# Performance work log

Hardware: AMD Instinct MI355X
Metric: run time of the kernel (lower is better)

Reference implementation:

```python
import jax, jax.numpy as jnp
import numpy as np

SEQ_LEN = 16
N_NODES = 64000
N_EDGES = 1024000
FEAT = 16
H1 = 64
H2 = 64
LSTM_DIM = 128
FC1 = 64
FC2 = 3


def setup_inputs() -> dict:
    key = jax.random.key(0)
    ks = jax.random.split(key, 16)
    def w(k, shape, fan_in):
        return (jax.random.normal(k, shape, jnp.float32) / np.float32(np.sqrt(fan_in)))
    return {
        "x": jax.random.normal(ks[0], (N_NODES, FEAT), jnp.float32),
        "edge_attr": jax.random.uniform(ks[1], (N_EDGES, 1), jnp.float32),
        "W1": w(ks[2], (FEAT, H1), FEAT),
        "b1": jnp.zeros((H1,), jnp.float32),
        "W2": w(ks[3], (H1, H2), H1),
        "b2": jnp.zeros((H2,), jnp.float32),
        "W_ih": w(ks[4], (4 * LSTM_DIM, H2), H2),
        "W_hh": w(ks[5], (4 * LSTM_DIM, LSTM_DIM), LSTM_DIM),
        "b_ih": jnp.zeros((4 * LSTM_DIM,), jnp.float32),
        "b_hh": jnp.zeros((4 * LSTM_DIM,), jnp.float32),
        "fw1": w(ks[6], (LSTM_DIM, FC1), LSTM_DIM),
        "fb1": jnp.zeros((FC1,), jnp.float32),
        "fw2": w(ks[7], (FC1, FC2), FC1),
        "fb2": jnp.zeros((FC2,), jnp.float32),
        "edge_index": jax.random.randint(ks[8], (2, N_EDGES), 0, N_NODES, dtype=jnp.int64),
        "batch_size": 8,
    }


def gcn_conv(x, edge_index, ew, W, b):
    # PyG GCNConv with edge_weight: add self-loops (weight 1), symmetric norm.
    n = x.shape[0]
    row, col = edge_index[0], edge_index[1]
    lin = x @ W                                        # [N, H]
    deg = jax.ops.segment_sum(ew, col, num_segments=n) + 1.0  # self-loop weight 1
    dinv = jax.lax.rsqrt(deg)
    norm = dinv[row] * ew * dinv[col]                  # [E]
    agg = jax.ops.segment_sum(norm[:, None] * lin[row], col, num_segments=n)
    agg = agg + lin * (dinv * dinv)[:, None]           # self-loop term: 1/deg
    return agg + b


def lstm_last(x, W_ih, W_hh, b_ih, b_hh):
    # x: [B, T, D]; torch LSTM gate order i, f, g, o. Returns last hidden [B, H].
    B = x.shape[0]
    H = W_hh.shape[1]
    xg = jnp.einsum('btd,gd->btg', x, W_ih) + (b_ih + b_hh)  # [B, T, 4H]
    def step(carry, g_t):
        h, c = carry
        g = g_t + h @ W_hh.T
        i, f, gg, o = jnp.split(g, 4, axis=-1)
        c = jax.nn.sigmoid(f) * c + jax.nn.sigmoid(i) * jnp.tanh(gg)
        h = jax.nn.sigmoid(o) * jnp.tanh(c)
        return (h, c), None
    h0 = jnp.zeros((B, H), x.dtype)
    (h, _), _ = jax.lax.scan(step, (h0, h0), xg.transpose(1, 0, 2))
    return h


def reference(x, edge_attr, W1, b1, W2, b2, W_ih, W_hh, b_ih, b_hh,
              fw1, fb1, fw2, fb2, edge_index, batch_size):
    ew = edge_attr[:, 0]
    out = gcn_conv(x, edge_index, ew, W1, b1)
    out = jax.nn.relu(out)                 # dropout: identity in eval
    out = gcn_conv(out, edge_index, ew, W2, b2)
    out = jax.nn.relu(out)
    out = out.reshape(-1, SEQ_LEN, out.shape[-1])      # [B*S, T, H2]
    h = lstm_last(out, W_ih, W_hh, b_ih, b_hh)          # [B*S, LSTM]
    h = h.reshape(batch_size, -1, LSTM_DIM)             # [B, S, LSTM]
    h = jax.nn.relu(h @ fw1 + fb1)
    logits = h @ fw2 + fb2
    return jax.nn.softmax(logits, axis=2)
```

## Files before the change

kernel.cpp:

```cpp
#include <hip/hip_runtime.h>
#include <hip/hip_bf16.h>
#include <hip/hip_fp16.h>
#include <math.h>

#define NN 64000
#define NE 1024000
#define NB 4000
#define NT 16
#define LROWS 16
#define NBKT 250

typedef __attribute__((ext_vector_type(8))) short short8;
typedef __attribute__((ext_vector_type(4))) float f32x4;

__device__ __forceinline__ float fsigm(float x) {
    return __builtin_amdgcn_rcpf(1.0f + __expf(-x));
}
__device__ __forceinline__ float ftanh(float x) {
    return 1.0f - 2.0f * __builtin_amdgcn_rcpf(1.0f + __expf(2.0f * x));
}
__device__ __forceinline__ unsigned short hbits(float v) {
    __half h = __float2half(v);
    return reinterpret_cast<unsigned short&>(h);
}
__device__ __forceinline__ float hval(unsigned short b) {
    __half h;
    reinterpret_cast<unsigned short&>(h) = b;
    return __half2float(h);
}

__global__ __launch_bounds__(256) void k_zero256(int* __restrict__ p) {
    p[threadIdx.x] = 0;
}

__global__ __launch_bounds__(256) void k_bhist(const int* __restrict__ ei,
                                               int* __restrict__ bcnt) {
    __shared__ int h[256];
    int tid = threadIdx.x;
    h[tid] = 0;
    __syncthreads();
    int base = blockIdx.x * 4096;
    #pragma unroll
    for (int j = 0; j < 16; ++j) {
        int c = ei[NE + base + j * 256 + tid];
        atomicAdd(&h[c >> 8], 1);
    }
    __syncthreads();
    if (tid < NBKT && h[tid]) atomicAdd(&bcnt[tid], h[tid]);
}

__global__ __launch_bounds__(256) void k_bscan(const int* __restrict__ bcnt,
                                               int* __restrict__ bbase,
                                               int* __restrict__ bcur) {
    __shared__ int sm[256];
    int tid = threadIdx.x;
    int v = (tid < NBKT) ? bcnt[tid] : 0;
    sm[tid] = v;
    __syncthreads();
    #pragma unroll
    for (int d = 1; d < 256; d <<= 1) {
        int t = (tid >= d) ? sm[tid - d] : 0;
        __syncthreads();
        sm[tid] += t;
        __syncthreads();
    }
    if (tid < NBKT) { int ex = sm[tid] - v; bbase[tid] = ex; bcur[tid] = ex; }
    if (tid == 255) bbase[NBKT] = sm[255];
}

__global__ __launch_bounds__(256) void k_bin(const int* __restrict__ ei,
                                             const float* __restrict__ ew,
                                             int* __restrict__ bcur,
                                             uint2* __restrict__ binned) {
    __shared__ uint2 stage[4096];
    __shared__ int sm[256];
    __shared__ int lofs[256], lcur[256], ladj[256];
    int tid = threadIdx.x;
    sm[tid] = 0;
    __syncthreads();
    int base = blockIdx.x * 4096;
    int cs[16];
    #pragma unroll
    for (int j = 0; j < 16; ++j) {
        cs[j] = ei[NE + base + j * 256 + tid];
        atomicAdd(&sm[cs[j] >> 8], 1);
    }
    __syncthreads();
    int v = sm[tid];
    #pragma unroll
    for (int d = 1; d < 256; d <<= 1) {
        int t = (tid >= d) ? sm[tid - d] : 0;
        __syncthreads();
        sm[tid] += t;
        __syncthreads();
    }
    int ex = sm[tid] - v;
    lofs[tid] = ex;
    lcur[tid] = ex;
    if (tid < NBKT) ladj[tid] = atomicAdd(&bcur[tid], v) - ex;
    __syncthreads();
    #pragma unroll
    for (int j = 0; j < 16; ++j) {
        int e = base + j * 256 + tid;
        int c = cs[j];
        int b = c >> 8;
        unsigned r = (unsigned)ei[e];
        float wv = ew[e];
        int slot = atomicAdd(&lcur[b], 1);
        stage[slot] = make_uint2(r | ((unsigned)(c & 255) << 16) | ((unsigned)b << 24),
                                 __float_as_uint(wv));
    }
    __syncthreads();
    #pragma unroll
    for (int j = 0; j < 16; ++j) {
        int i = j * 256 + tid;
        uint2 rec = stage[i];
        int b = rec.x >> 24;
        binned[ladj[b] + i] = rec;
    }
}

__global__ __launch_bounds__(256) void k_csr(const uint2* __restrict__ binned,
                                             const int* __restrict__ bbase,
                                             const float* __restrict__ x,
                                             unsigned* __restrict__ edata,
                                             int* __restrict__ off,
                                             float* __restrict__ dinv,
                                             __half* __restrict__ xh) {
    __shared__ int cnt[256];
    __shared__ float sumw[256];
    __shared__ int lcur[256];
    __shared__ int sm[256];
    int tid = threadIdx.x;
    int b = blockIdx.x;
    int s = bbase[b], e1 = bbase[b + 1];
    cnt[tid] = 0;
    sumw[tid] = 0.0f;
    __syncthreads();
    for (int i = s + tid; i < e1; i += 256) {
        uint2 rec = binned[i];
        int nl = (rec.x >> 16) & 255;
        atomicAdd(&cnt[nl], 1);
        atomicAdd(&sumw[nl], __uint_as_float(rec.y));
    }
    __syncthreads();
    int v = cnt[tid];
    sm[tid] = v;
    __syncthreads();
    #pragma unroll
    for (int d = 1; d < 256; d <<= 1) {
        int t = (tid >= d) ? sm[tid - d] : 0;
        __syncthreads();
        sm[tid] += t;
        __syncthreads();
    }
    int ex = sm[tid] - v;
    off[b * 256 + tid] = s + ex;
    float dv = rsqrtf(1.0f + sumw[tid]);
    dinv[b * 256 + tid] = dv;
    sumw[tid] = dv;
    lcur[tid] = ex;
    if (b == 0 && tid == 0) off[NN] = NE;
    __syncthreads();
    for (int i = s + tid; i < e1; i += 256) {
        uint2 rec = binned[i];
        int nl = (rec.x >> 16) & 255;
        int p = atomicAdd(&lcur[nl], 1);
        edata[s + p] = (rec.x & 0xFFFFu) |
                       ((unsigned)hbits(__uint_as_float(rec.y)) << 16);
    }
    size_t nb = (size_t)b * 4096;
    for (int i = tid; i < 4096; i += 256) {
        xh[nb + i] = __float2half(x[nb + i] * sumw[i >> 4]);
    }
}

__global__ __launch_bounds__(256) void k_gather16(const __half* __restrict__ xh,
                                                  const unsigned* __restrict__ edata,
                                                  const int* __restrict__ off,
                                                  const float* __restrict__ dinv,
                                                  __half* __restrict__ aggx) {
    int tid = threadIdx.x;
    int lane = tid & 63;
    int wv = tid >> 6;
    int n = blockIdx.x * 4 + wv;
    int g = lane >> 3;
    int fl = lane & 7;
    const __half2* xh2 = (const __half2*)xh;
    float2 acc = make_float2(0.0f, 0.0f);
    if (g == 0) acc = __half22float2(xh2[((size_t)n << 3) + fl]);
    int s = off[n], e1 = off[n + 1];
    int e = s + g;
    for (; e + 8 < e1; e += 16) {
        unsigned d0 = edata[e];
        unsigned d1 = edata[e + 8];
        float2 l0 = __half22float2(xh2[((size_t)(d0 & 0xFFFFu) << 3) + fl]);
        float2 l1 = __half22float2(xh2[((size_t)(d1 & 0xFFFFu) << 3) + fl]);
        float w0 = hval((unsigned short)(d0 >> 16));
        float w1 = hval((unsigned short)(d1 >> 16));
        acc.x = fmaf(w0, l0.x, acc.x); acc.y = fmaf(w0, l0.y, acc.y);
        acc.x = fmaf(w1, l1.x, acc.x); acc.y = fmaf(w1, l1.y, acc.y);
    }
    if (e < e1) {
        unsigned d0 = edata[e];
        float2 l0 = __half22float2(xh2[((size_t)(d0 & 0xFFFFu) << 3) + fl]);
        float w0 = hval((unsigned short)(d0 >> 16));
        acc.x = fmaf(w0, l0.x, acc.x);
        acc.y = fmaf(w0, l0.y, acc.y);
    }
    acc.x += __shfl_xor(acc.x, 8, 64);
    acc.y += __shfl_xor(acc.y, 8, 64);
    acc.x += __shfl_xor(acc.x, 16, 64);
    acc.y += __shfl_xor(acc.y, 16, 64);
    acc.x += __shfl_xor(acc.x, 32, 64);
    acc.y += __shfl_xor(acc.y, 32, 64);
    if (g == 0) {
        float dn = dinv[n];
        ((__half2*)aggx)[((size_t)n << 3) + fl] = __floats2half2_rn(dn * acc.x, dn * acc.y);
    }
}

__global__ __launch_bounds__(256) void k_wfrag(const float* __restrict__ W_ih,
                                               const float* __restrict__ W_hh,
                                               const float* __restrict__ b_ih,
                                               const float* __restrict__ b_hh,
                                               const float* __restrict__ W1,
                                               const float* __restrict__ W2,
                                               unsigned short* __restrict__ Bus,
                                               float* __restrict__ biasb,
                                               unsigned short* __restrict__ W1f,
                                               unsigned short* __restrict__ W2f) {
    int tid = threadIdx.x;
    int blk = blockIdx.x;
    if (blk < 384) {
        int i = blk * 256 + tid;
        if (i < 192 * 512) {
            int j = i & 7;
            int l = (i >> 3) & 63;
            int ci = i >> 9;
            int ntg = ci & 31;
            int ks = ci >> 5;
            int col = ntg * 16 + (l & 15);
            int k = ks * 32 + ((l >> 4) << 3) + j;
            float w = (k < 64) ? W_ih[col * 64 + k] : W_hh[col * 128 + (k - 64)];
            Bus[i] = hbits(w);
        }
        if (i < 512) biasb[i] = b_ih[i] + b_hh[i];
    } else {
        for (int i = tid; i < 6144; i += 256) {
            if (i < 2048) {
                int j = i & 7, l = (i >> 3) & 63, nt = i >> 9;
                int n = nt * 16 + (l & 15);
                int k = ((l >> 4) << 3) + j;
                W1f[i] = (k < 16) ? hbits(W1[k * 64 + n]) : (unsigned short)0;
            } else {
                int i2 = i - 2048;
                int j = i2 & 7, l = (i2 >> 3) & 63, ci = i2 >> 9;
                int nt = ci & 3, ks = ci >> 2;
                int n = nt * 16 + (l & 15);
                int k = ks * 32 + ((l >> 4) << 3) + j;
                W2f[i2] = hbits(W2[k * 64 + n]);
            }
        }
    }
}

__global__ __launch_bounds__(256) void k_lin2f(const __half* __restrict__ aggx,
                                               const unsigned short* __restrict__ W1f,
                                               const float* __restrict__ b1,
                                               const unsigned short* __restrict__ W2f,
                                               const float* __restrict__ dinv,
                                               __half* __restrict__ linp2) {
    __shared__ unsigned short Ax[4][512];
    __shared__ unsigned short Hd[4][2][512];
    __shared__ unsigned short Ot[64 * 64];
    int tid = threadIdx.x;
    int lane = tid & 63;
    int w = tid >> 6;
    int n0 = blockIdx.x * 64;

    short8 B1[4], B2[8];
    #pragma unroll
    for (int nt = 0; nt < 4; ++nt) B1[nt] = *(const short8*)&W1f[nt * 512 + lane * 8];
    #pragma unroll
    for (int ci = 0; ci < 8; ++ci) B2[ci] = *(const short8*)&W2f[ci * 512 + lane * 8];

    {
        int idx = tid;
        ((unsigned int*)Ax)[(idx >> 7) * 256 + 128 + (idx & 127)] = 0;
        idx += 256;
        ((unsigned int*)Ax)[(idx >> 7) * 256 + 128 + (idx & 127)] = 0;
    }
    {
        int row = tid >> 2, k0 = (tid & 3) * 4;
        uint2 bits = *(const uint2*)(aggx + (size_t)(n0 + row) * 16 + k0);
        unsigned short hv[4] = {(unsigned short)(bits.x & 0xFFFF), (unsigned short)(bits.x >> 16),
                                (unsigned short)(bits.y & 0xFFFF), (unsigned short)(bits.y >> 16)};
        int wq = row >> 4, m = row & 15;
        #pragma unroll
        for (int d = 0; d < 4; ++d) {
            int k = k0 + d;
            Ax[wq][(((k >> 3) << 4) + m) * 8 + (k & 7)] = hv[d];
        }
    }
    __syncthreads();

    short8 a = *(const short8*)&Ax[w][lane * 8];
    f32x4 acc[4];
    #pragma unroll
    for (int nt = 0; nt < 4; ++nt) acc[nt] = (f32x4){0.f, 0.f, 0.f, 0.f};
    #pragma unroll
    for (int nt = 0; nt < 4; ++nt)
        acc[nt] = __builtin_amdgcn_mfma_f32_16x16x32_f16(a, B1[nt], acc[nt], 0, 0, 0);

    int rb = (lane >> 4) * 4;
    #pragma unroll
    for (int nt = 0; nt < 4; ++nt) {
        int col = nt * 16 + (lane & 15);
        float bc = b1[col];
        #pragma unroll
        for (int q = 0; q < 4; ++q) {
            float hv = fmaxf(acc[nt][q] + bc, 0.0f);
            int row = rb + q;
            Hd[w][col >> 5][((((col & 31) >> 3) << 4) + row) * 8 + (col & 7)] = hbits(hv);
        }
    }
    short8 a0 = *(const short8*)&Hd[w][0][lane * 8];
    short8 a1 = *(const short8*)&Hd[w][1][lane * 8];
    f32x4 c2[4];
    #pragma unroll
    for (int nt = 0; nt < 4; ++nt) c2[nt] = (f32x4){0.f, 0.f, 0.f, 0.f};
    #pragma unroll
    for (int nt = 0; nt < 4; ++nt)
        c2[nt] = __builtin_amdgcn_mfma_f32_16x16x32_f16(a0, B2[nt], c2[nt], 0, 0, 0);
    #pragma unroll
    for (int nt = 0; nt < 4; ++nt)
        c2[nt] = __builtin_amdgcn_mfma_f32_16x16x32_f16(a1, B2[4 + nt], c2[nt], 0, 0, 0);

    float dv[4];
    #pragma unroll
    for (int q = 0; q < 4; ++q) dv[q] = dinv[n0 + w * 16 + rb + q];
    #pragma unroll
    for (int nt = 0; nt < 4; ++nt) {
        int col = nt * 16 + (lane & 15);
        #pragma unroll
        for (int q = 0; q < 4; ++q) {
            Ot[(w * 16 + rb + q) * 64 + col] = hbits(c2[nt][q] * dv[q]);
        }
    }
    __syncthreads();
    {
        int row = tid >> 2, c0 = (tid & 3) * 16;
        short8 v0 = *(const short8*)&Ot[row * 64 + c0];
        short8 v1 = *(const short8*)&Ot[row * 64 + c0 + 8];
        *(short8*)&linp2[(size_t)(n0 + row) * 64 + c0] = v0;
        *(short8*)&linp2[(size_t)(n0 + row) * 64 + c0 + 8] = v1;
    }
}

__global__ __launch_bounds__(256) void k_gather(const __half* __restrict__ linp,
                                                const unsigned* __restrict__ edata,
                                                const int* __restrict__ off,
                                                const float* __restrict__ dinv,
                                                const float* __restrict__ bvec,
                                                __half* __restrict__ agg) {
    int tid = threadIdx.x;
    int lane = tid & 63;
    int wv = tid >> 6;
    int n = blockIdx.x * 4 + wv;
    int hf = lane >> 5;
    int fl = lane & 31;
    const __half2* lp2 = (const __half2*)linp;
    float2 acc = make_float2(0.0f, 0.0f);
    if (hf == 0) {
        acc = __half22float2(lp2[((size_t)n << 5) + fl]);
    }
    int s = off[n], e1 = off[n + 1];
    int e = s + hf;
    for (; e + 6 < e1; e += 8) {
        unsigned d0 = edata[e];
        unsigned d1 = edata[e + 2];
        unsigned d2 = edata[e + 4];
        unsigned d3 = edata[e + 6];
        float2 l0 = __half22float2(lp2[((size_t)(d0 & 0xFFFFu) << 5) + fl]);
        float2 l1 = __half22float2(lp2[((size_t)(d1 & 0xFFFFu) << 5) + fl]);
        float2 l2 = __half22float2(lp2[((size_t)(d2 & 0xFFFFu) << 5) + fl]);
        float2 l3 = __half22float2(lp2[((size_t)(d3 & 0xFFFFu) << 5) + fl]);
        float w0 = hval((unsigned short)(d0 >> 16));
        float w1 = hval((unsigned short)(d1 >> 16));
        float w2 = hval((unsigned short)(d2 >> 16));
        float w3 = hval((unsigned short)(d3 >> 16));
        acc.x = fmaf(w0, l0.x, acc.x); acc.y = fmaf(w0, l0.y, acc.y);
        acc.x = fmaf(w1, l1.x, acc.x); acc.y = fmaf(w1, l1.y, acc.y);
        acc.x = fmaf(w2, l2.x, acc.x); acc.y = fmaf(w2, l2.y, acc.y);
        acc.x = fmaf(w3, l3.x, acc.x); acc.y = fmaf(w3, l3.y, acc.y);
    }
    for (; e < e1; e += 2) {
        unsigned d0 = edata[e];
        float2 l0 = __half22float2(lp2[((size_t)(d0 & 0xFFFFu) << 5) + fl]);
        float w0 = hval((unsigned short)(d0 >> 16));
        acc.x = fmaf(w0, l0.x, acc.x);
        acc.y = fmaf(w0, l0.y, acc.y);
    }
    acc.x += __shfl_xor(acc.x, 32, 64);
    acc.y += __shfl_xor(acc.y, 32, 64);
    if (hf == 0) {
        float dn = dinv[n];
        float ox = fmaxf(fmaf(dn, acc.x, bvec[fl * 2]), 0.0f);
        float oy = fmaxf(fmaf(dn, acc.y, bvec[fl * 2 + 1]), 0.0f);
        ((__half2*)agg)[((size_t)n << 5) + fl] = __floats2half2_rn(ox, oy);
    }
}

__global__ __launch_bounds__(512, 2) void k_lstm(const unsigned short* __restrict__ seq,
                                                 const unsigned short* __restrict__ Bus,
                                                 const float* __restrict__ biasb,
                                                 float* __restrict__ hout) {
    __shared__ unsigned short Aus[6 * 512];
    int tid = threadIdx.x;
    int lane = tid & 63;
    int w = tid >> 6;
    int b0 = blockIdx.x * LROWS;

    int u = w * 16 + (lane & 15);
    int rbase = (lane >> 4) * 4;
    float bI = biasb[u], bF = biasb[128 + u], bG = biasb[256 + u], bO = biasb[384 + u];
    float cst[4] = {0.0f, 0.0f, 0.0f, 0.0f};

    short8 Bf[24];
    #pragma unroll
    for (int ks = 0; ks < 6; ++ks) {
        #pragma unroll
        for (int g = 0; g < 4; ++g) {
            int ci = ks * 32 + 8 * g + w;
            Bf[ks * 4 + g] = *(const short8*)&Bus[(size_t)ci * 512 + lane * 8];
        }
    }

    for (int i = tid; i < 1024; i += 512) ((unsigned int*)Aus)[512 + i] = 0;
    {
        int i0 = tid * 2;
        int row = i0 >> 6, k0 = i0 & 63;
        unsigned v = *(const unsigned*)&seq[((size_t)(b0 + row) * NT + 0) * 64 + k0];
        int ks = k0 >> 5, kr = k0 & 31;
        Aus[ks * 512 + (((kr >> 3) << 4) + row) * 8 + (kr & 7)] = (unsigned short)v;
        kr = (k0 + 1) & 31; ks = (k0 + 1) >> 5;
        Aus[ks * 512 + (((kr >> 3) << 4) + row) * 8 + (kr & 7)] = (unsigned short)(v >> 16);
    }
    __syncthreads();

    for (int t = 0; t < NT; ++t) {
        f32x4 acc[4];
        #pragma unroll
        for (int g = 0; g < 4; ++g) acc[g] = (f32x4){0.f, 0.f, 0.f, 0.f};
        #pragma unroll
        for (int ks = 0; ks < 6; ++ks) {
            short8 ah = *(const short8*)&Aus[ks * 512 + lane * 8];
            #pragma unroll
            for (int g = 0; g < 4; ++g)
                acc[g] = __builtin_amdgcn_mfma_f32_16x16x32_f16(ah, Bf[ks * 4 + g], acc[g], 0, 0, 0);
        }
        __syncthreads();

        if (t == NT - 1) {
            #pragma unroll
            for (int q = 0; q < 4; ++q) {
                float nc = fsigm(acc[1][q] + bF) * cst[q]
                         + fsigm(acc[0][q] + bI) * ftanh(acc[2][q] + bG);
                cst[q] = nc;
                float hv = fsigm(acc[3][q] + bO) * ftanh(nc);
                hout[(size_t)(b0 + rbase + q) * 128 + u] = hv;
            }
        } else {
            int kh = 64 + u;
            int ksh = kh >> 5, krh = kh & 31;
            int hbase = ksh * 512 + ((krh >> 3) << 4) * 8 + (krh & 7);
            #pragma unroll
            for (int q = 0; q < 4; ++q) {
                float nc = fsigm(acc[1][q] + bF) * cst[q]
                         + fsigm(acc[0][q] + bI) * ftanh(acc[2][q] + bG);
                cst[q] = nc;
                float hv = fsigm(acc[3][q] + bO) * ftanh(nc);
                Aus[hbase + (rbase + q) * 8] = hbits(hv);
            }
            {
                int i0 = tid * 2;
                int row = i0 >> 6, k0 = i0 & 63;
                unsigned v = *(const unsigned*)&seq[((size_t)(b0 + row) * NT + (t + 1)) * 64 + k0];
                int ks = k0 >> 5, kr = k0 & 31;
                Aus[ks * 512 + (((kr >> 3) << 4) + row) * 8 + (kr & 7)] = (unsigned short)v;
                kr = (k0 + 1) & 31; ks = (k0 + 1) >> 5;
                Aus[ks * 512 + (((kr >> 3) << 4) + row) * 8 + (kr & 7)] = (unsigned short)(v >> 16);
            }
            __syncthreads();
        }
    }
}

__global__ __launch_bounds__(256) void k_fc(const float* __restrict__ h,
                                            const float* __restrict__ fw1,
                                            const float* __restrict__ fb1,
                                            const float* __restrict__ fw2,
                                            const float* __restrict__ fb2,
                                            float* __restrict__ out) {
    __shared__ float hid[4][64];
    int tid = threadIdx.x;
    int lane = tid & 63;
    int w = tid >> 6;
    int b = blockIdx.x * 4 + w;
    const float* hr = h + b * 128;
    float acc = fb1[lane];
    #pragma unroll 4
    for (int k = 0; k < 128; ++k) acc = fmaf(hr[k], fw1[k * 64 + lane], acc);
    hid[w][lane] = fmaxf(acc, 0.0f);
    __syncthreads();
    if (lane == 0) {
        float lg[3];
        #pragma unroll
        for (int l = 0; l < 3; ++l) {
            float a = fb2[l];
            for (int j = 0; j < 64; ++j) a = fmaf(hid[w][j], fw2[j * 3 + l], a);
            lg[l] = a;
        }
        float m = fmaxf(lg[0], fmaxf(lg[1], lg[2]));
        float e0 = expf(lg[0] - m), e1 = expf(lg[1] - m), e2 = expf(lg[2] - m);
        float s = 1.0f / (e0 + e1 + e2);
        out[b * 3 + 0] = e0 * s;
        out[b * 3 + 1] = e1 * s;
        out[b * 3 + 2] = e2 * s;
    }
}

extern "C" void kernel_launch(void* const* d_in, const int* in_sizes, int n_in,
                              void* d_out, int out_size, void* d_ws, size_t ws_size,
                              hipStream_t stream) {
    const float* x    = (const float*)d_in[0];
    const float* ea   = (const float*)d_in[1];
    const float* W1   = (const float*)d_in[2];
    const float* b1   = (const float*)d_in[3];
    const float* W2   = (const float*)d_in[4];
    const float* b2   = (const float*)d_in[5];
    const float* W_ih = (const float*)d_in[6];
    const float* W_hh = (const float*)d_in[7];
    const float* b_ih = (const float*)d_in[8];
    const float* b_hh = (const float*)d_in[9];
    const float* fw1  = (const float*)d_in[10];
    const float* fb1  = (const float*)d_in[11];
    const float* fw2  = (const float*)d_in[12];
    const float* fb2  = (const float*)d_in[13];
    const int*   ei   = (const int*)d_in[14];
    float* out = (float*)d_out;

    float* ws    = (float*)d_ws;
    float* dinv  = ws;
    float* bufA  = dinv + NN;
    float* bufB  = bufA + NN * 64;
    unsigned short* Bus = (unsigned short*)(bufB + NN * 64);
    float* biasb = bufB + NN * 64 + 98304 / 2;
    float* hbuf  = biasb + 512;
    int*   bcnt  = (int*)(hbuf + NB * 128);
    int*   bbase = bcnt + 256;
    int*   bcur  = bbase + 256;
    int*   off   = bcur + 256;
    unsigned* edata = (unsigned*)(off + NN + 4);
    __half* aggx = (__half*)(edata + NE);
    __half* xh   = aggx + NN * 16;
    unsigned short* W1f = (unsigned short*)(xh + NN * 16);
    unsigned short* W2f = W1f + 2048;
    uint2* binned = (uint2*)bufA;
    __half* linp  = (__half*)bufA;
    __half* aggB  = (__half*)bufB;

    k_zero256<<<1, 256, 0, stream>>>(bcnt);
    k_bhist<<<NBKT, 256, 0, stream>>>(ei, bcnt);
    k_bscan<<<1, 256, 0, stream>>>(bcnt, bbase, bcur);
    k_bin<<<NBKT, 256, 0, stream>>>(ei, ea, bcur, binned);
    k_csr<<<NBKT, 256, 0, stream>>>(binned, bbase, x, edata, off, dinv, xh);

    k_wfrag<<<385, 256, 0, stream>>>(W_ih, W_hh, b_ih, b_hh, W1, W2, Bus, biasb, W1f, W2f);

    k_gather16<<<16000, 256, 0, stream>>>(xh, edata, off, dinv, aggx);

    k_lin2f<<<1000, 256, 0, stream>>>(aggx, W1f, b1, W2f, dinv, linp);

    k_gather<<<16000, 256, 0, stream>>>(linp, edata, off, dinv, b2, aggB);

    k_lstm<<<250, 512, 0, stream>>>((const unsigned short*)aggB, Bus, biasb, hbuf);

    k_fc<<<1000, 256, 0, stream>>>(hbuf, fw1, fb1, fw2, fb2, out);
}
```

Baseline: 154.3 us.

## Fuse FC head into LSTM, double-buffer LSTM input, fold zeroing into weight prep

The FC+softmax head now runs inside the LSTM kernel: final hidden states are kept in shared memory, fw1 is staged into LDS, and each block writes its 16 output rows directly. This removes the k_fc launch and the hbuf round trip. The LSTM A-operand buffer is double-buffered, so each timestep needs one barrier instead of two. The zeroing of bucket counts moves into an extra block of k_wfrag, which now runs first, removing the k_zero256 launch. Shared memory use per LSTM block rises by roughly 48KB, which may limit occupancy.

```diff
diff --git a/kernel.cpp b/kernel.cpp
--- a/kernel.cpp
+++ b/kernel.cpp
@@ -27,10 +27,6 @@
     __half h;
     reinterpret_cast<unsigned short&>(h) = b;
     return __half2float(h);
-}
-
-__global__ __launch_bounds__(256) void k_zero256(int* __restrict__ p) {
-    p[threadIdx.x] = 0;
 }
 
 __global__ __launch_bounds__(256) void k_bhist(const int* __restrict__ ei,
@@ -229,7 +225,8 @@
                                                unsigned short* __restrict__ Bus,
                                                float* __restrict__ biasb,
                                                unsigned short* __restrict__ W1f,
-                                               unsigned short* __restrict__ W2f) {
+                                               unsigned short* __restrict__ W2f,
+                                               int* __restrict__ bcnt) {
     int tid = threadIdx.x;
     int blk = blockIdx.x;
     if (blk < 384) {
@@ -246,7 +243,7 @@
             Bus[i] = hbits(w);
         }
         if (i < 512) biasb[i] = b_ih[i] + b_hh[i];
-    } else {
+    } else if (blk == 384) {
         for (int i = tid; i < 6144; i += 256) {
             if (i < 2048) {
                 int j = i & 7, l = (i >> 3) & 63, nt = i >> 9;
@@ -262,6 +259,8 @@
                 W2f[i2] = hbits(W2[k * 64 + n]);
             }
         }
+    } else {
+        bcnt[tid] = 0;
     }
 }
 
@@ -415,8 +414,15 @@
 __global__ __launch_bounds__(512, 2) void k_lstm(const unsigned short* __restrict__ seq,
                                                  const unsigned short* __restrict__ Bus,
                                                  const float* __restrict__ biasb,
-                                                 float* __restrict__ hout) {
-    __shared__ unsigned short Aus[6 * 512];
+                                                 const float* __restrict__ fw1,
+                                                 const float* __restrict__ fb1,
+                                                 const float* __restrict__ fw2,
+                                                 const float* __restrict__ fb2,
+                                                 float* __restrict__ out) {
+    __shared__ unsigned short Aus[2][6 * 512];
+    __shared__ float fw1s[128 * 64];
+    __shared__ float hsm[16][128];
+    __shared__ float hid2[16][64];
     int tid = threadIdx.x;
     int lane = tid & 63;
     int w = tid >> 6;
@@ -437,39 +443,39 @@
         }
     }
 
-    for (int i = tid; i < 1024; i += 512) ((unsigned int*)Aus)[512 + i] = 0;
+    for (int i = tid; i < 128 * 64; i += 512) fw1s[i] = fw1[i];
+
+    for (int i = tid; i < 1024; i += 512) ((unsigned int*)Aus[0])[512 + i] = 0;
     {
         int i0 = tid * 2;
         int row = i0 >> 6, k0 = i0 & 63;
         unsigned v = *(const unsigned*)&seq[((size_t)(b0 + row) * NT + 0) * 64 + k0];
         int ks = k0 >> 5, kr = k0 & 31;
-        Aus[ks * 512 + (((kr >> 3) << 4) + row) * 8 + (kr & 7)] = (unsigned short)v;
+        Aus[0][ks * 512 + (((kr >> 3) << 4) + row) * 8 + (kr & 7)] = (unsigned short)v;
         kr = (k0 + 1) & 31; ks = (k0 + 1) >> 5;
-        Aus[ks * 512 + (((kr >> 3) << 4) + row) * 8 + (kr & 7)] = (unsigned short)(v >> 16);
-    }
-    __syncthreads();
-
+        Aus[0][ks * 512 + (((kr >> 3) << 4) + row) * 8 + (kr & 7)] = (unsigned short)(v >> 16);
+    }
+    __syncthreads();
+
+    int p = 0;
     for (int t = 0; t < NT; ++t) {
         f32x4 acc[4];
         #pragma unroll
         for (int g = 0; g < 4; ++g) acc[g] = (f32x4){0.f, 0.f, 0.f, 0.f};
         #pragma unroll
         for (int ks = 0; ks < 6; ++ks) {
-            short8 ah = *(const short8*)&Aus[ks * 512 + lane * 8];
+            short8 ah = *(const short8*)&Aus[p][ks * 512 + lane * 8];
             #pragma unroll
             for (int g = 0; g < 4; ++g)
                 acc[g] = __builtin_amdgcn_mfma_f32_16x16x32_f16(ah, Bf[ks * 4 + g], acc[g], 0, 0, 0);
         }
-        __syncthreads();
-
         if (t == NT - 1) {
             #pragma unroll
             for (int q = 0; q < 4; ++q) {
                 float nc = fsigm(acc[1][q] + bF) * cst[q]
                          + fsigm(acc[0][q] + bI) * ftanh(acc[2][q] + bG);
                 cst[q] = nc;
-                float hv = fsigm(acc[3][q] + bO) * ftanh(nc);
-                hout[(size_t)(b0 + rbase + q) * 128 + u] = hv;
+                hsm[rbase + q][u] = fsigm(acc[3][q] + bO) * ftanh(nc);
             }
         } else {
             int kh = 64 + u;
@@ -481,53 +487,51 @@
                          + fsigm(acc[0][q] + bI) * ftanh(acc[2][q] + bG);
                 cst[q] = nc;
                 float hv = fsigm(acc[3][q] + bO) * ftanh(nc);
-                Aus[hbase + (rbase + q) * 8] = hbits(hv);
+                Aus[p ^ 1][hbase + (rbase + q) * 8] = hbits(hv);
             }
             {
                 int i0 = tid * 2;
                 int row = i0 >> 6, k0 = i0 & 63;
                 unsigned v = *(const unsigned*)&seq[((size_t)(b0 + row) * NT + (t + 1)) * 64 + k0];
                 int ks = k0 >> 5, kr = k0 & 31;
-                Aus[ks * 512 + (((kr >> 3) << 4) + row) * 8 + (kr & 7)] = (unsigned short)v;
+                Aus[p ^ 1][ks * 512 + (((kr >> 3) << 4) + row) * 8 + (kr & 7)] = (unsigned short)v;
                 kr = (k0 + 1) & 31; ks = (k0 + 1) >> 5;
-                Aus[ks * 512 + (((kr >> 3) << 4) + row) * 8 + (kr & 7)] = (unsigned short)(v >> 16);
+                Aus[p ^ 1][ks * 512 + (((kr >> 3) << 4) + row) * 8 + (kr & 7)] = (unsigned short)(v >> 16);
             }
-            __syncthreads();
-        }
-    }
-}
-
-__global__ __launch_bounds__(256) void k_fc(const float* __restrict__ h,
-                                            const float* __restrict__ fw1,
-                                            const float* __restrict__ fb1,
-                                            const float* __restrict__ fw2,
-                                            const float* __restrict__ fb2,
-                                            float* __restrict__ out) {
-    __shared__ float hid[4][64];
-    int tid = threadIdx.x;
-    int lane = tid & 63;
-    int w = tid >> 6;
-    int b = blockIdx.x * 4 + w;
-    const float* hr = h + b * 128;
-    float acc = fb1[lane];
-    #pragma unroll 4
-    for (int k = 0; k < 128; ++k) acc = fmaf(hr[k], fw1[k * 64 + lane], acc);
-    hid[w][lane] = fmaxf(acc, 0.0f);
-    __syncthreads();
-    if (lane == 0) {
+        }
+        __syncthreads();
+        p ^= 1;
+    }
+
+    {
+        int row = tid >> 5;
+        int f0 = (tid & 31) * 2;
+        float a0 = fb1[f0], a1 = fb1[f0 + 1];
+        #pragma unroll 8
+        for (int k = 0; k < 128; ++k) {
+            float hk = hsm[row][k];
+            a0 = fmaf(hk, fw1s[k * 64 + f0], a0);
+            a1 = fmaf(hk, fw1s[k * 64 + f0 + 1], a1);
+        }
+        hid2[row][f0] = fmaxf(a0, 0.0f);
+        hid2[row][f0 + 1] = fmaxf(a1, 0.0f);
+    }
+    __syncthreads();
+    if (tid < 16) {
         float lg[3];
         #pragma unroll
         for (int l = 0; l < 3; ++l) {
             float a = fb2[l];
-            for (int j = 0; j < 64; ++j) a = fmaf(hid[w][j], fw2[j * 3 + l], a);
+            for (int j = 0; j < 64; ++j) a = fmaf(hid2[tid][j], fw2[j * 3 + l], a);
             lg[l] = a;
         }
         float m = fmaxf(lg[0], fmaxf(lg[1], lg[2]));
         float e0 = expf(lg[0] - m), e1 = expf(lg[1] - m), e2 = expf(lg[2] - m);
         float s = 1.0f / (e0 + e1 + e2);
-        out[b * 3 + 0] = e0 * s;
-        out[b * 3 + 1] = e1 * s;
-        out[b * 3 + 2] = e2 * s;
+        size_t ob = (size_t)(b0 + tid) * 3;
+        out[ob + 0] = e0 * s;
+        out[ob + 1] = e1 * s;
+        out[ob + 2] = e2 * s;
     }
 }
 
@@ -557,8 +561,7 @@
     float* bufB  = bufA + NN * 64;
     unsigned short* Bus = (unsigned short*)(bufB + NN * 64);
     float* biasb = bufB + NN * 64 + 98304 / 2;
-    float* hbuf  = biasb + 512;
-    int*   bcnt  = (int*)(hbuf + NB * 128);
+    int*   bcnt  = (int*)(biasb + 512);
     int*   bbase = bcnt + 256;
     int*   bcur  = bbase + 256;
     int*   off   = bcur + 256;
@@ -571,21 +574,19 @@
     __half* linp  = (__half*)bufA;
     __half* aggB  = (__half*)bufB;
 
-    k_zero256<<<1, 256, 0, stream>>>(bcnt);
+    k_wfrag<<<386, 256, 0, stream>>>(W_ih, W_hh, b_ih, b_hh, W1, W2, Bus, biasb, W1f, W2f, bcnt);
+
     k_bhist<<<NBKT, 256, 0, stream>>>(ei, bcnt);
     k_bscan<<<1, 256, 0, stream>>>(bcnt, bbase, bcur);
     k_bin<<<NBKT, 256, 0, stream>>>(ei, ea, bcur, binned);
     k_csr<<<NBKT, 256, 0, stream>>>(binned, bbase, x, edata, off, dinv, xh);
 
-    k_wfrag<<<385, 256, 0, stream>>>(W_ih, W_hh, b_ih, b_hh, W1, W2, Bus, biasb, W1f, W2f);
-
     k_gather16<<<16000, 256, 0, stream>>>(xh, edata, off, dinv, aggx);
 
     k_lin2f<<<1000, 256, 0, stream>>>(aggx, W1f, b1, W2f, dinv, linp);
 
     k_gather<<<16000, 256, 0, stream>>>(linp, edata, off, dinv, b2, aggB);
 
-    k_lstm<<<250, 512, 0, stream>>>((const unsigned short*)aggB, Bus, biasb, hbuf);
-
-    k_fc<<<1000, 256, 0, stream>>>(hbuf, fw1, fb1, fw2, fb2, out);
-}
+    k_lstm<<<250, 512, 0, stream>>>((const unsigned short*)aggB, Bus, biasb,
+                                    fw1, fb1, fw2, fb2, out);
+}
```

New measurement: 140.9 us. 8.7% less time.
